# Optimization experiments

Measured on AMD Instinct MI355X. Metric: run time of the kernel, lower is better.

Reference implementation:

```python
import jax, jax.numpy as jnp
from jax import lax
import numpy as np

# Layer dims: (in, hidden) for encoder 1-3 and decoder 1-3
INPUT_SIZE = 64
HIDDEN_SIZE = 16
LAYER_DIMS = [
    ("e1", INPUT_SIZE, 48), ("e2", 48, 32), ("e3", 32, HIDDEN_SIZE),
    ("d1", HIDDEN_SIZE, 32), ("d2", 32, 48), ("d3", 48, INPUT_SIZE),
]


def _lstm_layer(x, Wih, Whh, bih, bhh):
    """PyTorch-convention single-layer LSTM (gate order i,f,g,o), batch_first.
    x: [B,T,D], Wih: [4H,D], Whh: [4H,H], biases: [4H].
    Returns (outputs [B,T,H], last_h [B,H])."""
    B, T, _ = x.shape
    H = Whh.shape[1]
    # Precompute input contribution to all gates for all timesteps (one big GEMM).
    xg = jnp.einsum('btd,gd->btg', x, Wih) + (bih + bhh)  # [B,T,4H]

    def step(carry, xt):
        h, c = carry
        g = xt + h @ Whh.T                      # [B,4H]
        i, f, gg, o = jnp.split(g, 4, axis=-1)
        i = jax.nn.sigmoid(i)
        f = jax.nn.sigmoid(f)
        gg = jnp.tanh(gg)
        o = jax.nn.sigmoid(o)
        c = f * c + i * gg
        h = o * jnp.tanh(c)
        return (h, c), h

    h0 = jnp.zeros((B, H), x.dtype)
    (hT, _), ys = lax.scan(step, (h0, h0), jnp.swapaxes(xg, 0, 1))
    return jnp.swapaxes(ys, 0, 1), hT


def setup_inputs() -> dict:
    key = jax.random.key(0)
    B, T = 512, 512
    k_x, key = jax.random.split(key)
    inp = {"x": jax.random.normal(k_x, (B, T, INPUT_SIZE), dtype=jnp.float32)}
    for name, din, dh in LAYER_DIMS:
        bound = 1.0 / np.sqrt(dh)  # PyTorch nn.LSTM init: U(-1/sqrt(H), 1/sqrt(H))
        for suf, shape in [("Wih", (4 * dh, din)), ("Whh", (4 * dh, dh)),
                           ("bih", (4 * dh,)), ("bhh", (4 * dh,))]:
            key, k = jax.random.split(key)
            inp[f"{name}_{suf}"] = jax.random.uniform(
                k, shape, minval=-bound, maxval=bound, dtype=jnp.float32)
    return inp


def reference(x,
              e1_Wih, e1_Whh, e1_bih, e1_bhh,
              e2_Wih, e2_Whh, e2_bih, e2_bhh,
              e3_Wih, e3_Whh, e3_bih, e3_bhh,
              d1_Wih, d1_Whh, d1_bih, d1_bhh,
              d2_Wih, d2_Whh, d2_bih, d2_bhh,
              d3_Wih, d3_Whh, d3_bih, d3_bhh):
    # Encoder
    z, _ = _lstm_layer(x, e1_Wih, e1_Whh, e1_bih, e1_bhh)
    z, _ = _lstm_layer(z, e2_Wih, e2_Whh, e2_bih, e2_bhh)
    _, last_h = _lstm_layer(z, e3_Wih, e3_Whh, e3_bih, e3_bhh)
    # Repeat latent across time: [B,H] -> [B,T,H]
    T = x.shape[1]
    x_enc = jnp.broadcast_to(last_h[:, None, :], (x.shape[0], T, last_h.shape[-1]))
    # Decoder
    z, _ = _lstm_layer(x_enc, d1_Wih, d1_Whh, d1_bih, d1_bhh)
    z, _ = _lstm_layer(z, d2_Wih, d2_Whh, d2_bih, d2_bhh)
    x_dec, _ = _lstm_layer(z, d3_Wih, d3_Whh, d3_bih, d3_bhh)
    return x_dec
```

## Files before the change

### kernel.cpp

```cpp
#include <hip/hip_runtime.h>
#include <hip/hip_bf16.h>
#include <cstdint>
#include <cstddef>

typedef _Float16 half_t;
typedef decltype(__builtin_amdgcn_cvt_pkrtz(0.f, 0.f)) h2;

__device__ __forceinline__ h2 pk2(float a, float b) { return __builtin_amdgcn_cvt_pkrtz(a, b); }
__device__ __forceinline__ float fdot2f(h2 a, h2 b, float c) { return __builtin_amdgcn_fdot2(a, b, c, false); }
__device__ __forceinline__ h2 u2h(uint32_t u) { union { uint32_t u; h2 h; } v; v.u = u; return v.h; }

#define WAVE_SYNC() asm volatile("s_waitcnt lgkmcnt(0)" ::: "memory")
#define BLOCK_SYNC()                                   \
  do {                                                 \
    asm volatile("s_waitcnt lgkmcnt(0)" ::: "memory"); \
    __builtin_amdgcn_s_barrier();                      \
    asm volatile("" ::: "memory");                     \
  } while (0)

template <int NQ>
__device__ __forceinline__ void fetch_q(const half_t* hb, uint4* q) {
  const uint4* p = (const uint4*)hb;
#pragma unroll
  for (int i = 0; i < NQ; ++i) q[i] = p[i];
}

template <int NQ>
__device__ __forceinline__ void dot2acc(const h2* w, const uint4* q, float& a0, float& a1) {
#pragma unroll
  for (int i = 0; i < NQ; ++i) {
    a0 = fdot2f(w[4 * i + 0], u2h(q[i].x), a0);
    a1 = fdot2f(w[4 * i + 1], u2h(q[i].y), a1);
    a0 = fdot2f(w[4 * i + 2], u2h(q[i].z), a0);
    a1 = fdot2f(w[4 * i + 3], u2h(q[i].w), a1);
  }
}

__device__ __forceinline__ void load_row_h2(const float* src, int nf, h2* dst) {
  const float2* s2 = (const float2*)src;
  for (int p = 0; p < nf / 2; ++p) { float2 v = s2[p]; dst[p] = pk2(v.x, v.y); }
}

__device__ __forceinline__ void gconst(int gt, float& s, float& a, float& b) {
  const bool isT = (gt == 2);
  s = isT ? -2.88539008f : -1.44269504f;
  a = isT ? 2.f : 1.f;
  b = isT ? -1.f : 0.f;
}

__device__ __forceinline__ float act_sig(float x) {
  float e = exp2f(-1.44269504f * x);
  return __builtin_amdgcn_rcpf(1.f + e);
}
__device__ __forceinline__ float act_tanh(float x) {
  float e = exp2f(-2.88539008f * x);
  return fmaf(2.f, __builtin_amdgcn_rcpf(1.f + e), -1.f);
}
__device__ __forceinline__ float act_rt(float x, float s, float a, float b) {
  float e = exp2f(s * x);
  return fmaf(a, __builtin_amdgcn_rcpf(1.f + e), b);
}

__device__ __forceinline__ float comb4(float gi, float gf, float gg, float go, float& c) {
  c = fmaf(gf, c, gi * gg);
  float e2 = exp2f(-2.88539008f * c);
  return go * fmaf(2.f, __builtin_amdgcn_rcpf(1.f + e2), -1.f);
}

__device__ __forceinline__ float pair_combine(float gv0, float gv1, int l, float& c) {
  float sw0 = __shfl_xor(gv0, 32, 64);
  float sw1 = __shfl_xor(gv1, 32, 64);
  const bool lo = (l < 32);
  float gi = lo ? gv0 : sw0, gf = lo ? gv1 : sw1;
  float gg = lo ? sw0 : gv0, go = lo ? sw1 : gv1;
  return comb4(gi, gf, gg, go, c);
}

__global__ __launch_bounds__(256, 2) void enc_ker(
    const float* __restrict__ W0, const float* __restrict__ U0, const float* __restrict__ b0i, const float* __restrict__ b0h,
    const float* __restrict__ W1, const float* __restrict__ U1, const float* __restrict__ b1i, const float* __restrict__ b1h,
    const float* __restrict__ W2, const float* __restrict__ U2, const float* __restrict__ b2i, const float* __restrict__ b2h,
    const float* __restrict__ x, float* __restrict__ lat, int T) {
  __shared__ __align__(16) half_t hb1[2][48];
  __shared__ __align__(16) half_t hb2[2][32];
  __shared__ __align__(16) half_t hb3[2][16];
  __shared__ __align__(16) uint32_t xrow16[2][32];
  __shared__ __align__(16) float xg1[2][192];

  const int tid = threadIdx.x, wv = tid >> 6, l = tid & 63, b = blockIdx.x;
  const int uu = (l < 48) ? l : 47;

  if (tid < 48) { hb1[0][tid] = (half_t)0.f; hb1[1][tid] = (half_t)0.f; }
  if (tid < 32) { hb2[0][tid] = (half_t)0.f; hb2[1][tid] = (half_t)0.f; }
  if (tid < 16) { hb3[0][tid] = (half_t)0.f; hb3[1][tid] = (half_t)0.f; }

  h2 w[96];
  float bias[3] = {0.f, 0.f, 0.f};
  float sA[2], aA[2], bB[2];
  float c = 0.f;
  float2 va = {0.f, 0.f}, vb = {0.f, 0.f};
  const float2* xp = nullptr;

  if (wv == 0) {
#pragma unroll
    for (int j = 0; j < 4; ++j)
      load_row_h2(U0 + (size_t)(j * 48 + uu) * 48, 48, w + j * 24);
  } else if (wv == 1) {
    const int u = l & 31, g0 = (l < 32) ? 0 : 2;
#pragma unroll
    for (int j = 0; j < 2; ++j) {
      const int r = (g0 + j) * 32 + u;
      load_row_h2(W1 + (size_t)r * 48, 48, w + j * 40);
      load_row_h2(U1 + (size_t)r * 32, 32, w + j * 40 + 24);
      bias[j] = b1i[r] + b1h[r];
      gconst(g0 + j, sA[j], aA[j], bB[j]);
    }
  } else if (wv == 2) {
    load_row_h2(W2 + (size_t)l * 32, 32, w);
    load_row_h2(U2 + (size_t)l * 16, 16, w + 16);
    bias[0] = b2i[l] + b2h[l];
    gconst(l >> 4, sA[0], aA[0], bB[0]);
  } else {
#pragma unroll
    for (int j = 0; j < 3; ++j) {
      const int r = 64 * j + l;
      load_row_h2(W0 + (size_t)r * 64, 64, w + j * 32);
      bias[j] = b0i[r] + b0h[r];
    }
    xp = (const float2*)(x + (size_t)b * T * 64) + (l & 31);
    if (l < 32) {
      float2 x0 = xp[0], x1 = xp[32];
      union { h2 h; uint32_t u; } c0, c1;
      c0.h = pk2(x0.x, x0.y);
      c1.h = pk2(x1.x, x1.y);
      xrow16[0][l] = c0.u;
      xrow16[1][l] = c1.u;
      va = xp[64];
      vb = xp[96];
    }
    WAVE_SYNC();
    uint4 xq[8];
    const uint4* xr = (const uint4*)&xrow16[0][0];
#pragma unroll
    for (int i = 0; i < 8; ++i) xq[i] = xr[i];
#pragma unroll
    for (int j = 0; j < 3; ++j) {
      float a0 = bias[j], a1 = 0.f;
      dot2acc<8>(w + j * 32, xq, a0, a1);
      xg1[0][64 * j + l] = a0 + a1;
    }
  }
  BLOCK_SYNC();

  auto estep = [&](int s, int P) {
    const int Q = P ^ 1;
    if (wv == 0) {
      if (s < T) {
        float xgv[4];
#pragma unroll
        for (int j = 0; j < 4; ++j) xgv[j] = xg1[P][j * 48 + uu];
        uint4 hq[6];
        fetch_q<6>(&hb1[Q][0], hq);
        float gv[4];
#pragma unroll
        for (int j = 0; j < 4; ++j) {
          float a0 = xgv[j], a1 = 0.f;
          dot2acc<6>(w + j * 24, hq, a0, a1);
          gv[j] = (j == 2) ? act_tanh(a0 + a1) : act_sig(a0 + a1);
        }
        float h = comb4(gv[0], gv[1], gv[2], gv[3], c);
        if (l < 48) hb1[P][l] = (half_t)h;
      }
    } else if (wv == 1) {
      if (s >= 1 && s <= T) {
        uint4 xv[6], hq[4];
        fetch_q<6>(&hb1[Q][0], xv);
        fetch_q<4>(&hb2[Q][0], hq);
        float gv[2];
#pragma unroll
        for (int j = 0; j < 2; ++j) {
          float a0 = bias[j], a1 = 0.f;
          dot2acc<6>(w + j * 40, xv, a0, a1);
          dot2acc<4>(w + j * 40 + 24, hq, a0, a1);
          gv[j] = act_rt(a0 + a1, sA[j], aA[j], bB[j]);
        }
        float h = pair_combine(gv[0], gv[1], l, c);
        if (l < 32) hb2[P][l & 31] = (half_t)h;
      }
    } else if (wv == 2) {
      if (s >= 2) {
        uint4 xv[4], hq[2];
        fetch_q<4>(&hb2[Q][0], xv);
        fetch_q<2>(&hb3[Q][0], hq);
        float a0 = bias[0], a1 = 0.f;
        dot2acc<4>(w, xv, a0, a1);
        dot2acc<2>(w + 16, hq, a0, a1);
        float gvv = act_rt(a0 + a1, sA[0], aA[0], bB[0]);
        float s1 = __shfl_xor(gvv, 16, 64);
        float r0 = __shfl_xor(gvv, 32, 64);
        float r1 = __shfl_xor(s1, 32, 64);
        float h = comb4(gvv, s1, r0, r1, c);
        if (l < 16) {
          hb3[P][l] = (half_t)h;
          if (s - 2 == T - 1) lat[(size_t)b * 16 + l] = h;
        }
      }
    } else {
      if (s + 2 < T && l < 32) {
        union { h2 h; uint32_t u; } cc2;
        float2 v = P ? vb : va;
        cc2.h = pk2(v.x, v.y);
        xrow16[P][l] = cc2.u;
        if (s + 4 < T) {
          float2 nv = xp[(size_t)(s + 4) * 32];
          if (P) vb = nv; else va = nv;
        }
      }
      if (s + 1 < T) {
        WAVE_SYNC();
        uint4 xq[8];
        const uint4* xr = (const uint4*)&xrow16[Q][0];
#pragma unroll
        for (int i = 0; i < 8; ++i) xq[i] = xr[i];
#pragma unroll
        for (int j = 0; j < 3; ++j) {
          float a0 = bias[j], a1 = 0.f;
          dot2acc<8>(w + j * 32, xq, a0, a1);
          xg1[Q][64 * j + l] = a0 + a1;
        }
      }
    }
    BLOCK_SYNC();
  };

  const int NS = T + 2;
  for (int sb = 0; sb < NS; sb += 2) {
    estep(sb, 0);
    estep(sb + 1, 1);
  }
}

__global__ __launch_bounds__(256, 2) void dec_ker(
    const float* __restrict__ W3, const float* __restrict__ U3, const float* __restrict__ b3i, const float* __restrict__ b3h,
    const float* __restrict__ W4, const float* __restrict__ U4, const float* __restrict__ b4i, const float* __restrict__ b4h,
    const float* __restrict__ W5, const float* __restrict__ U5, const float* __restrict__ b5i, const float* __restrict__ b5h,
    const float* __restrict__ lat, float* __restrict__ out, int T) {
  __shared__ __align__(16) half_t hb1[2][32];
  __shared__ __align__(16) half_t hb2[2][48];
  __shared__ __align__(16) half_t hb3[2][64];
  __shared__ __align__(16) float xg2[2][192];

  const int tid = threadIdx.x, wv = tid >> 6, l = tid & 63, b = blockIdx.x;
  const int uu = (l < 48) ? l : 47;

  if (tid < 32) { hb1[0][tid] = (half_t)0.f; hb1[1][tid] = (half_t)0.f; }
  if (tid < 48) { hb2[0][tid] = (half_t)0.f; hb2[1][tid] = (half_t)0.f; }
  if (tid < 64) { hb3[0][tid] = (half_t)0.f; hb3[1][tid] = (half_t)0.f; }

  h2 w[112];
  float bias[3] = {0.f, 0.f, 0.f};
  float bx[3] = {0.f, 0.f, 0.f};
  float sA[2], aA[2], bB[2];
  float c = 0.f;
  const int u2 = (l & 31) + ((wv == 3) ? 32 : 0);

  if (wv == 0) {
    const int u = l & 31, g0 = (l < 32) ? 0 : 2;
    const float* lt = lat + (size_t)b * 16;
#pragma unroll
    for (int j = 0; j < 2; ++j) {
      const int r = (g0 + j) * 32 + u;
      load_row_h2(U3 + (size_t)r * 32, 32, w + j * 16);
      float s0 = b3i[r] + b3h[r];
      const float* wr = W3 + (size_t)r * 16;
#pragma unroll
      for (int d = 0; d < 16; ++d) s0 = fmaf(wr[d], lt[d], s0);
      bias[j] = s0;
      gconst(g0 + j, sA[j], aA[j], bB[j]);
    }
#pragma unroll
    for (int jj = 0; jj < 3; ++jj) {
      const int r = 64 * jj + l;
      load_row_h2(W4 + (size_t)r * 32, 32, w + 32 + jj * 16);
      bx[jj] = b4i[r] + b4h[r];
    }
  } else if (wv == 1) {
#pragma unroll
    for (int j = 0; j < 4; ++j)
      load_row_h2(U4 + (size_t)(j * 48 + uu) * 48, 48, w + j * 24);
  } else {
    const int g0 = (l < 32) ? 0 : 2;
#pragma unroll
    for (int j = 0; j < 2; ++j) {
      const int r = (g0 + j) * 64 + u2;
      load_row_h2(W5 + (size_t)r * 48, 48, w + j * 56);
      load_row_h2(U5 + (size_t)r * 64, 64, w + j * 56 + 24);
      bias[j] = b5i[r] + b5h[r];
      gconst(g0 + j, sA[j], aA[j], bB[j]);
    }
  }
  BLOCK_SYNC();

  auto dstep = [&](int s, int P) {
    const int Q = P ^ 1;
    if (wv == 0) {
      if (s <= T) {
        uint4 hq[4];
        fetch_q<4>(&hb1[Q][0], hq);
        if (s < T) {
          float gv[2];
#pragma unroll
          for (int j = 0; j < 2; ++j) {
            float a0 = bias[j], a1 = 0.f;
            dot2acc<4>(w + j * 16, hq, a0, a1);
            gv[j] = act_rt(a0 + a1, sA[j], aA[j], bB[j]);
          }
          float h = pair_combine(gv[0], gv[1], l, c);
          if (l < 32) hb1[P][l & 31] = (half_t)h;
        }
        if (s >= 1) {
#pragma unroll
          for (int jj = 0; jj < 3; ++jj) {
            float a0 = bx[jj], a1 = 0.f;
            dot2acc<4>(w + 32 + jj * 16, hq, a0, a1);
            xg2[P][64 * jj + l] = a0 + a1;
          }
        }
      }
    } else if (wv == 1) {
      if (s >= 2 && s < T + 2) {
        float xgv[4];
#pragma unroll
        for (int j = 0; j < 4; ++j) xgv[j] = xg2[Q][j * 48 + uu];
        uint4 hq[6];
        fetch_q<6>(&hb2[Q][0], hq);
        float gv[4];
#pragma unroll
        for (int j = 0; j < 4; ++j) {
          float a0 = xgv[j], a1 = 0.f;
          dot2acc<6>(w + j * 24, hq, a0, a1);
          gv[j] = (j == 2) ? act_tanh(a0 + a1) : act_sig(a0 + a1);
        }
        float h = comb4(gv[0], gv[1], gv[2], gv[3], c);
        if (l < 48) hb2[P][l] = (half_t)h;
      }
    } else {
      if (s >= 3) {
        const int t = s - 3;
        if (t < T) {
          uint4 xv[6], hq[8];
          fetch_q<6>(&hb2[Q][0], xv);
          fetch_q<8>(&hb3[Q][0], hq);
          float gv[2];
#pragma unroll
          for (int j = 0; j < 2; ++j) {
            float a0 = bias[j], a1 = 0.f;
            dot2acc<6>(w + j * 56, xv, a0, a1);
            dot2acc<8>(w + j * 56 + 24, hq, a0, a1);
            gv[j] = act_rt(a0 + a1, sA[j], aA[j], bB[j]);
          }
          float h = pair_combine(gv[0], gv[1], l, c);
          if (l < 32) {
            hb3[P][u2] = (half_t)h;
            out[((size_t)b * T + t) * 64 + u2] = h;
          }
        }
      }
    }
    BLOCK_SYNC();
  };

  const int NS = T + 4;
  for (int sb = 0; sb < NS; sb += 2) {
    dstep(sb, 0);
    dstep(sb + 1, 1);
  }
}

extern "C" void kernel_launch(void* const* d_in, const int* in_sizes, int n_in,
                              void* d_out, int out_size, void* d_ws, size_t ws_size,
                              hipStream_t stream) {
  (void)in_sizes; (void)n_in; (void)out_size; (void)ws_size;
  const float* x = (const float*)d_in[0];
  const float *W[6], *U[6], *Bi[6], *Bh[6];
  for (int lyr = 0; lyr < 6; ++lyr) {
    W[lyr]  = (const float*)d_in[1 + 4 * lyr + 0];
    U[lyr]  = (const float*)d_in[1 + 4 * lyr + 1];
    Bi[lyr] = (const float*)d_in[1 + 4 * lyr + 2];
    Bh[lyr] = (const float*)d_in[1 + 4 * lyr + 3];
  }
  float* out = (float*)d_out;
  const int T = 512;
  float* lat = (float*)d_ws;

  enc_ker<<<dim3(512), dim3(256), 0, stream>>>(
      W[0], U[0], Bi[0], Bh[0], W[1], U[1], Bi[1], Bh[1], W[2], U[2], Bi[2], Bh[2],
      x, lat, T);
  dec_ker<<<dim3(512), dim3(256), 0, stream>>>(
      W[3], U[3], Bi[3], Bh[3], W[4], U[4], Bi[4], Bh[4], W[5], U[5], Bi[5], Bh[5],
      lat, out, T);
}
```

Baseline: 791.9 us.

## Fuse encoder and decoder into one kernel with guard-free steady-state loops

Merges the encoder and decoder kernels into a single kernel. The latent vector now passes through shared memory instead of global workspace, which removes one launch and the global round trip. It also splits each step loop into guarded prologue and epilogue steps plus a steady-state loop that has no bounds checks. Dot products now use four independent accumulators instead of two to shorten the dependency chain, and s_setprio is raised around the critical matvecs. The main risks are higher register and LDS pressure in the fused kernel, which may hurt occupancy, and a steady-state loop that hard-codes T=512.

```diff
diff --git a/kernel.cpp b/kernel.cpp
--- a/kernel.cpp
+++ b/kernel.cpp
@@ -26,13 +26,13 @@
 }
 
 template <int NQ>
-__device__ __forceinline__ void dot2acc(const h2* w, const uint4* q, float& a0, float& a1) {
+__device__ __forceinline__ void dot4(const h2* w, const uint4* q, float* a) {
 #pragma unroll
   for (int i = 0; i < NQ; ++i) {
-    a0 = fdot2f(w[4 * i + 0], u2h(q[i].x), a0);
-    a1 = fdot2f(w[4 * i + 1], u2h(q[i].y), a1);
-    a0 = fdot2f(w[4 * i + 2], u2h(q[i].z), a0);
-    a1 = fdot2f(w[4 * i + 3], u2h(q[i].w), a1);
+    a[0] = fdot2f(w[4 * i + 0], u2h(q[i].x), a[0]);
+    a[1] = fdot2f(w[4 * i + 1], u2h(q[i].y), a[1]);
+    a[2] = fdot2f(w[4 * i + 2], u2h(q[i].z), a[2]);
+    a[3] = fdot2f(w[4 * i + 3], u2h(q[i].w), a[3]);
   }
 }
 
@@ -76,26 +76,35 @@
   return comb4(gi, gf, gg, go, c);
 }
 
-__global__ __launch_bounds__(256, 2) void enc_ker(
+__global__ __launch_bounds__(256, 2) void ae_ker(
     const float* __restrict__ W0, const float* __restrict__ U0, const float* __restrict__ b0i, const float* __restrict__ b0h,
     const float* __restrict__ W1, const float* __restrict__ U1, const float* __restrict__ b1i, const float* __restrict__ b1h,
     const float* __restrict__ W2, const float* __restrict__ U2, const float* __restrict__ b2i, const float* __restrict__ b2h,
-    const float* __restrict__ x, float* __restrict__ lat, int T) {
-  __shared__ __align__(16) half_t hb1[2][48];
-  __shared__ __align__(16) half_t hb2[2][32];
-  __shared__ __align__(16) half_t hb3[2][16];
+    const float* __restrict__ W3, const float* __restrict__ U3, const float* __restrict__ b3i, const float* __restrict__ b3h,
+    const float* __restrict__ W4, const float* __restrict__ U4, const float* __restrict__ b4i, const float* __restrict__ b4h,
+    const float* __restrict__ W5, const float* __restrict__ U5, const float* __restrict__ b5i, const float* __restrict__ b5h,
+    const float* __restrict__ x, float* __restrict__ out, int T) {
+  __shared__ __align__(16) half_t hb1e[2][48];
+  __shared__ __align__(16) half_t hb2e[2][32];
+  __shared__ __align__(16) half_t hb3e[2][16];
   __shared__ __align__(16) uint32_t xrow16[2][32];
   __shared__ __align__(16) float xg1[2][192];
+  __shared__ __align__(16) float latb[16];
+  __shared__ __align__(16) half_t hb1d[2][32];
+  __shared__ __align__(16) half_t hb2d[2][48];
+  __shared__ __align__(16) half_t hb3d[2][64];
+  __shared__ __align__(16) float xg2[2][192];
 
   const int tid = threadIdx.x, wv = tid >> 6, l = tid & 63, b = blockIdx.x;
   const int uu = (l < 48) ? l : 47;
 
-  if (tid < 48) { hb1[0][tid] = (half_t)0.f; hb1[1][tid] = (half_t)0.f; }
-  if (tid < 32) { hb2[0][tid] = (half_t)0.f; hb2[1][tid] = (half_t)0.f; }
-  if (tid < 16) { hb3[0][tid] = (half_t)0.f; hb3[1][tid] = (half_t)0.f; }
-
-  h2 w[96];
+  if (tid < 48) { hb1e[0][tid] = (half_t)0.f; hb1e[1][tid] = (half_t)0.f; }
+  if (tid < 32) { hb2e[0][tid] = (half_t)0.f; hb2e[1][tid] = (half_t)0.f; }
+  if (tid < 16) { hb3e[0][tid] = (half_t)0.f; hb3e[1][tid] = (half_t)0.f; }
+
+  h2 w[112];
   float bias[3] = {0.f, 0.f, 0.f};
+  float bx[3] = {0.f, 0.f, 0.f};
   float sA[2], aA[2], bB[2];
   float c = 0.f;
   float2 va = {0.f, 0.f}, vb = {0.f, 0.f};
@@ -145,128 +154,114 @@
     for (int i = 0; i < 8; ++i) xq[i] = xr[i];
 #pragma unroll
     for (int j = 0; j < 3; ++j) {
-      float a0 = bias[j], a1 = 0.f;
-      dot2acc<8>(w + j * 32, xq, a0, a1);
-      xg1[0][64 * j + l] = a0 + a1;
+      float a[4] = {bias[j], 0.f, 0.f, 0.f};
+      dot4<8>(w + j * 32, xq, a);
+      xg1[0][64 * j + l] = (a[0] + a[1]) + (a[2] + a[3]);
     }
   }
   BLOCK_SYNC();
 
-  auto estep = [&](int s, int P) {
+  auto estep = [&](const bool G, int s, int P) {
     const int Q = P ^ 1;
     if (wv == 0) {
-      if (s < T) {
+      if (!G || s < T) {
         float xgv[4];
 #pragma unroll
         for (int j = 0; j < 4; ++j) xgv[j] = xg1[P][j * 48 + uu];
         uint4 hq[6];
-        fetch_q<6>(&hb1[Q][0], hq);
+        fetch_q<6>(&hb1e[Q][0], hq);
+        __builtin_amdgcn_s_setprio(1);
         float gv[4];
 #pragma unroll
         for (int j = 0; j < 4; ++j) {
-          float a0 = xgv[j], a1 = 0.f;
-          dot2acc<6>(w + j * 24, hq, a0, a1);
-          gv[j] = (j == 2) ? act_tanh(a0 + a1) : act_sig(a0 + a1);
-        }
+          float a[4] = {xgv[j], 0.f, 0.f, 0.f};
+          dot4<6>(w + j * 24, hq, a);
+          float pre = (a[0] + a[1]) + (a[2] + a[3]);
+          gv[j] = (j == 2) ? act_tanh(pre) : act_sig(pre);
+        }
+        __builtin_amdgcn_s_setprio(0);
         float h = comb4(gv[0], gv[1], gv[2], gv[3], c);
-        if (l < 48) hb1[P][l] = (half_t)h;
+        if (l < 48) hb1e[P][l] = (half_t)h;
       }
     } else if (wv == 1) {
-      if (s >= 1 && s <= T) {
+      if (!G || (s >= 1 && s <= T)) {
         uint4 xv[6], hq[4];
-        fetch_q<6>(&hb1[Q][0], xv);
-        fetch_q<4>(&hb2[Q][0], hq);
+        fetch_q<6>(&hb1e[Q][0], xv);
+        fetch_q<4>(&hb2e[Q][0], hq);
         float gv[2];
 #pragma unroll
         for (int j = 0; j < 2; ++j) {
-          float a0 = bias[j], a1 = 0.f;
-          dot2acc<6>(w + j * 40, xv, a0, a1);
-          dot2acc<4>(w + j * 40 + 24, hq, a0, a1);
-          gv[j] = act_rt(a0 + a1, sA[j], aA[j], bB[j]);
+          float a[4] = {bias[j], 0.f, 0.f, 0.f};
+          dot4<6>(w + j * 40, xv, a);
+          dot4<4>(w + j * 40 + 24, hq, a);
+          gv[j] = act_rt((a[0] + a[1]) + (a[2] + a[3]), sA[j], aA[j], bB[j]);
         }
         float h = pair_combine(gv[0], gv[1], l, c);
-        if (l < 32) hb2[P][l & 31] = (half_t)h;
+        if (l < 32) hb2e[P][l & 31] = (half_t)h;
       }
     } else if (wv == 2) {
-      if (s >= 2) {
+      if (!G || s >= 2) {
         uint4 xv[4], hq[2];
-        fetch_q<4>(&hb2[Q][0], xv);
-        fetch_q<2>(&hb3[Q][0], hq);
-        float a0 = bias[0], a1 = 0.f;
-        dot2acc<4>(w, xv, a0, a1);
-        dot2acc<2>(w + 16, hq, a0, a1);
-        float gvv = act_rt(a0 + a1, sA[0], aA[0], bB[0]);
+        fetch_q<4>(&hb2e[Q][0], xv);
+        fetch_q<2>(&hb3e[Q][0], hq);
+        float a[4] = {bias[0], 0.f, 0.f, 0.f};
+        dot4<4>(w, xv, a);
+        dot4<2>(w + 16, hq, a);
+        float gvv = act_rt((a[0] + a[1]) + (a[2] + a[3]), sA[0], aA[0], bB[0]);
         float s1 = __shfl_xor(gvv, 16, 64);
         float r0 = __shfl_xor(gvv, 32, 64);
         float r1 = __shfl_xor(s1, 32, 64);
         float h = comb4(gvv, s1, r0, r1, c);
         if (l < 16) {
-          hb3[P][l] = (half_t)h;
-          if (s - 2 == T - 1) lat[(size_t)b * 16 + l] = h;
+          hb3e[P][l] = (half_t)h;
+          if (G && s - 2 == T - 1) latb[l] = h;
         }
       }
     } else {
-      if (s + 2 < T && l < 32) {
+      if ((!G || s + 2 < T) && l < 32) {
         union { h2 h; uint32_t u; } cc2;
         float2 v = P ? vb : va;
         cc2.h = pk2(v.x, v.y);
         xrow16[P][l] = cc2.u;
-        if (s + 4 < T) {
+        if (!G || s + 4 < T) {
           float2 nv = xp[(size_t)(s + 4) * 32];
           if (P) vb = nv; else va = nv;
         }
       }
-      if (s + 1 < T) {
+      if (!G || s + 1 < T) {
         WAVE_SYNC();
         uint4 xq[8];
         const uint4* xr = (const uint4*)&xrow16[Q][0];
 #pragma unroll
         for (int i = 0; i < 8; ++i) xq[i] = xr[i];
+        __builtin_amdgcn_s_setprio(1);
 #pragma unroll
         for (int j = 0; j < 3; ++j) {
-          float a0 = bias[j], a1 = 0.f;
-          dot2acc<8>(w + j * 32, xq, a0, a1);
-          xg1[Q][64 * j + l] = a0 + a1;
-        }
+          float a[4] = {bias[j], 0.f, 0.f, 0.f};
+          dot4<8>(w + j * 32, xq, a);
+          xg1[Q][64 * j + l] = (a[0] + a[1]) + (a[2] + a[3]);
+        }
+        __builtin_amdgcn_s_setprio(0);
       }
     }
     BLOCK_SYNC();
   };
 
-  const int NS = T + 2;
-  for (int sb = 0; sb < NS; sb += 2) {
-    estep(sb, 0);
-    estep(sb + 1, 1);
-  }
-}
-
-__global__ __launch_bounds__(256, 2) void dec_ker(
-    const float* __restrict__ W3, const float* __restrict__ U3, const float* __restrict__ b3i, const float* __restrict__ b3h,
-    const float* __restrict__ W4, const float* __restrict__ U4, const float* __restrict__ b4i, const float* __restrict__ b4h,
-    const float* __restrict__ W5, const float* __restrict__ U5, const float* __restrict__ b5i, const float* __restrict__ b5h,
-    const float* __restrict__ lat, float* __restrict__ out, int T) {
-  __shared__ __align__(16) half_t hb1[2][32];
-  __shared__ __align__(16) half_t hb2[2][48];
-  __shared__ __align__(16) half_t hb3[2][64];
-  __shared__ __align__(16) float xg2[2][192];
-
-  const int tid = threadIdx.x, wv = tid >> 6, l = tid & 63, b = blockIdx.x;
-  const int uu = (l < 48) ? l : 47;
-
-  if (tid < 32) { hb1[0][tid] = (half_t)0.f; hb1[1][tid] = (half_t)0.f; }
-  if (tid < 48) { hb2[0][tid] = (half_t)0.f; hb2[1][tid] = (half_t)0.f; }
-  if (tid < 64) { hb3[0][tid] = (half_t)0.f; hb3[1][tid] = (half_t)0.f; }
-
-  h2 w[112];
-  float bias[3] = {0.f, 0.f, 0.f};
-  float bx[3] = {0.f, 0.f, 0.f};
-  float sA[2], aA[2], bB[2];
-  float c = 0.f;
+  {
+    const int NS = T + 2;
+    for (int s = 0; s < 4; ++s) estep(true, s, s & 1);
+    for (int s = 4; s < 508; s += 2) { estep(false, s, 0); estep(false, s + 1, 1); }
+    for (int s = 508; s < NS; ++s) estep(true, s, s & 1);
+  }
+
+  c = 0.f;
+  if (tid < 32) { hb1d[0][tid] = (half_t)0.f; hb1d[1][tid] = (half_t)0.f; }
+  if (tid < 48) { hb2d[0][tid] = (half_t)0.f; hb2d[1][tid] = (half_t)0.f; }
+  if (tid < 64) { hb3d[0][tid] = (half_t)0.f; hb3d[1][tid] = (half_t)0.f; }
   const int u2 = (l & 31) + ((wv == 3) ? 32 : 0);
 
   if (wv == 0) {
     const int u = l & 31, g0 = (l < 32) ? 0 : 2;
-    const float* lt = lat + (size_t)b * 16;
 #pragma unroll
     for (int j = 0; j < 2; ++j) {
       const int r = (g0 + j) * 32 + u;
@@ -274,7 +269,7 @@
       float s0 = b3i[r] + b3h[r];
       const float* wr = W3 + (size_t)r * 16;
 #pragma unroll
-      for (int d = 0; d < 16; ++d) s0 = fmaf(wr[d], lt[d], s0);
+      for (int d = 0; d < 16; ++d) s0 = fmaf(wr[d], latb[d], s0);
       bias[j] = s0;
       gconst(g0 + j, sA[j], aA[j], bB[j]);
     }
@@ -301,86 +296,89 @@
   }
   BLOCK_SYNC();
 
-  auto dstep = [&](int s, int P) {
+  auto dstep = [&](const bool G, int s, int P) {
     const int Q = P ^ 1;
     if (wv == 0) {
-      if (s <= T) {
+      if (!G || s <= T) {
         uint4 hq[4];
-        fetch_q<4>(&hb1[Q][0], hq);
-        if (s < T) {
+        fetch_q<4>(&hb1d[Q][0], hq);
+        if (!G || s < T) {
           float gv[2];
 #pragma unroll
           for (int j = 0; j < 2; ++j) {
-            float a0 = bias[j], a1 = 0.f;
-            dot2acc<4>(w + j * 16, hq, a0, a1);
-            gv[j] = act_rt(a0 + a1, sA[j], aA[j], bB[j]);
+            float a[4] = {bias[j], 0.f, 0.f, 0.f};
+            dot4<4>(w + j * 16, hq, a);
+            gv[j] = act_rt((a[0] + a[1]) + (a[2] + a[3]), sA[j], aA[j], bB[j]);
           }
           float h = pair_combine(gv[0], gv[1], l, c);
-          if (l < 32) hb1[P][l & 31] = (half_t)h;
-        }
-        if (s >= 1) {
+          if (l < 32) hb1d[P][l & 31] = (half_t)h;
+        }
+        if (!G || s >= 1) {
 #pragma unroll
           for (int jj = 0; jj < 3; ++jj) {
-            float a0 = bx[jj], a1 = 0.f;
-            dot2acc<4>(w + 32 + jj * 16, hq, a0, a1);
-            xg2[P][64 * jj + l] = a0 + a1;
+            float a[4] = {bx[jj], 0.f, 0.f, 0.f};
+            dot4<4>(w + 32 + jj * 16, hq, a);
+            xg2[P][64 * jj + l] = (a[0] + a[1]) + (a[2] + a[3]);
           }
         }
       }
     } else if (wv == 1) {
-      if (s >= 2 && s < T + 2) {
+      if (!G || (s >= 2 && s < T + 2)) {
         float xgv[4];
 #pragma unroll
         for (int j = 0; j < 4; ++j) xgv[j] = xg2[Q][j * 48 + uu];
         uint4 hq[6];
-        fetch_q<6>(&hb2[Q][0], hq);
+        fetch_q<6>(&hb2d[Q][0], hq);
+        __builtin_amdgcn_s_setprio(1);
         float gv[4];
 #pragma unroll
         for (int j = 0; j < 4; ++j) {
-          float a0 = xgv[j], a1 = 0.f;
-          dot2acc<6>(w + j * 24, hq, a0, a1);
-          gv[j] = (j == 2) ? act_tanh(a0 + a1) : act_sig(a0 + a1);
-        }
+          float a[4] = {xgv[j], 0.f, 0.f, 0.f};
+          dot4<6>(w + j * 24, hq, a);
+          float pre = (a[0] + a[1]) + (a[2] + a[3]);
+          gv[j] = (j == 2) ? act_tanh(pre) : act_sig(pre);
+        }
+        __builtin_amdgcn_s_setprio(0);
         float h = comb4(gv[0], gv[1], gv[2], gv[3], c);
-        if (l < 48) hb2[P][l] = (half_t)h;
+        if (l < 48) hb2d[P][l] = (half_t)h;
       }
     } else {
-      if (s >= 3) {
-        const int t = s - 3;
-        if (t < T) {
-          uint4 xv[6], hq[8];
-          fetch_q<6>(&hb2[Q][0], xv);
-          fetch_q<8>(&hb3[Q][0], hq);
-          float gv[2];
-#pragma unroll
-          for (int j = 0; j < 2; ++j) {
-            float a0 = bias[j], a1 = 0.f;
-            dot2acc<6>(w + j * 56, xv, a0, a1);
-            dot2acc<8>(w + j * 56 + 24, hq, a0, a1);
-            gv[j] = act_rt(a0 + a1, sA[j], aA[j], bB[j]);
-          }
-          float h = pair_combine(gv[0], gv[1], l, c);
-          if (l < 32) {
-            hb3[P][u2] = (half_t)h;
-            out[((size_t)b * T + t) * 64 + u2] = h;
-          }
+      if (!G || (s >= 3 && s < T + 3)) {
+        uint4 xv[6], hq[8];
+        fetch_q<6>(&hb2d[Q][0], xv);
+        fetch_q<8>(&hb3d[Q][0], hq);
+        __builtin_amdgcn_s_setprio(1);
+        float gv[2];
+#pragma unroll
+        for (int j = 0; j < 2; ++j) {
+          float a[4] = {bias[j], 0.f, 0.f, 0.f};
+          dot4<6>(w + j * 56, xv, a);
+          dot4<8>(w + j * 56 + 24, hq, a);
+          gv[j] = act_rt((a[0] + a[1]) + (a[2] + a[3]), sA[j], aA[j], bB[j]);
+        }
+        __builtin_amdgcn_s_setprio(0);
+        float h = pair_combine(gv[0], gv[1], l, c);
+        if (l < 32) {
+          hb3d[P][u2] = (half_t)h;
+          out[((size_t)b * T + (s - 3)) * 64 + u2] = h;
         }
       }
     }
     BLOCK_SYNC();
   };
 
-  const int NS = T + 4;
-  for (int sb = 0; sb < NS; sb += 2) {
-    dstep(sb, 0);
-    dstep(sb + 1, 1);
+  {
+    const int NS = T + 4;
+    for (int s = 0; s < 4; ++s) dstep(true, s, s & 1);
+    for (int s = 4; s < 508; s += 2) { dstep(false, s, 0); dstep(false, s + 1, 1); }
+    for (int s = 508; s < NS; ++s) dstep(true, s, s & 1);
   }
 }
 
 extern "C" void kernel_launch(void* const* d_in, const int* in_sizes, int n_in,
                               void* d_out, int out_size, void* d_ws, size_t ws_size,
                               hipStream_t stream) {
-  (void)in_sizes; (void)n_in; (void)out_size; (void)ws_size;
+  (void)in_sizes; (void)n_in; (void)out_size; (void)d_ws; (void)ws_size;
   const float* x = (const float*)d_in[0];
   const float *W[6], *U[6], *Bi[6], *Bh[6];
   for (int lyr = 0; lyr < 6; ++lyr) {
@@ -391,12 +389,9 @@
   }
   float* out = (float*)d_out;
   const int T = 512;
-  float* lat = (float*)d_ws;
-
-  enc_ker<<<dim3(512), dim3(256), 0, stream>>>(
+
+  ae_ker<<<dim3(512), dim3(256), 0, stream>>>(
       W[0], U[0], Bi[0], Bh[0], W[1], U[1], Bi[1], Bh[1], W[2], U[2], Bi[2], Bh[2],
-      x, lat, T);
-  dec_ker<<<dim3(512), dim3(256), 0, stream>>>(
       W[3], U[3], Bi[3], Bh[3], W[4], U[4], Bi[4], Bh[4], W[5], U[5], Bi[5], Bh[5],
-      lat, out, T);
-}
+      x, out, T);
+}
```

Result: faster. 723.7 us (median of 3 runs) (-8.6%).
